# Kernel optimization log

Measured on AMD Instinct MI355X. Metric: run time of the kernel, lower is better.

## Reference

```python
import jax, jax.numpy as jnp
import numpy as np

B, C, N, M = 16, 256, 4096, 1024
EPS = 1e-5


def geometry_disentangle(x, num_select):
    # x: [B, C, N]. Variation score = L2 norm of mean-centered feature per point.
    score = jnp.linalg.norm(x - x.mean(axis=2, keepdims=True), axis=1)  # [B, N]
    _, idx_s = jax.lax.top_k(score, num_select)    # sharp: highest variation
    _, idx_g = jax.lax.top_k(-score, num_select)   # gentle: lowest variation
    sharp = jnp.take_along_axis(x, idx_s[:, None, :], axis=2)   # [B, C, M]
    gentle = jnp.take_along_axis(x, idx_g[:, None, :], axis=2)  # [B, C, M]
    return sharp, gentle


def cross_attention(x, ctx, Wq, bq, Wk, bk, Wv, bv, Wo, bo):
    # x: [B, C, N], ctx: [B, M, C] -> [B, C, N]
    c = x.shape[1]
    q = jnp.einsum('bcn,dc->bdn', x, Wq) + bq[None, :, None]  # conv1x1 on x
    k = jnp.einsum('bmc,dc->bmd', ctx, Wk) + bk
    v = jnp.einsum('bmc,dc->bmd', ctx, Wv) + bv
    scores = jnp.einsum('bdn,bmd->bnm', q, k) / jnp.sqrt(jnp.asarray(c, x.dtype))
    attn = jax.nn.softmax(scores, axis=-1)                     # [B, N, M]
    y = jnp.einsum('bnm,bmd->bdn', attn, v)                    # [B, C, N]
    y = jnp.einsum('bdn,ed->ben', y, Wo) + bo[None, :, None]   # output conv1x1
    return x + y


def conv_bn_relu(h, Wf, bf, gamma, beta):
    # Conv1d(k=1) + BatchNorm1d (training-mode batch stats) + ReLU. h: [B, 2C, N]
    y = jnp.einsum('bcn,dc->bdn', h, Wf) + bf[None, :, None]   # [B, C, N]
    mu = y.mean(axis=(0, 2), keepdims=True)
    var = y.var(axis=(0, 2), keepdims=True)
    y = (y - mu) * jax.lax.rsqrt(var + EPS)
    y = y * gamma[None, :, None] + beta[None, :, None]
    return jax.nn.relu(y)


def setup_inputs() -> dict:
    key = jax.random.key(0)
    ks = jax.random.split(key, 20)
    s = 0.02

    def w(k, shape):
        return (jax.random.normal(k, shape, dtype=jnp.float32) * s)

    inp = {
        'x': jax.random.normal(ks[0], (B, C, N), dtype=jnp.float32),
        'num_select': M,
        # sharp attention params
        'Wq_s': w(ks[1], (C, C)), 'bq_s': jnp.zeros((C,), jnp.float32),
        'Wk_s': w(ks[2], (C, C)), 'bk_s': jnp.zeros((C,), jnp.float32),
        'Wv_s': w(ks[3], (C, C)), 'bv_s': jnp.zeros((C,), jnp.float32),
        'Wo_s': w(ks[4], (C, C)), 'bo_s': jnp.zeros((C,), jnp.float32),
        # gentle attention params
        'Wq_g': w(ks[5], (C, C)), 'bq_g': jnp.zeros((C,), jnp.float32),
        'Wk_g': w(ks[6], (C, C)), 'bk_g': jnp.zeros((C,), jnp.float32),
        'Wv_g': w(ks[7], (C, C)), 'bv_g': jnp.zeros((C,), jnp.float32),
        'Wo_g': w(ks[8], (C, C)), 'bo_g': jnp.zeros((C,), jnp.float32),
        # fuse: Conv1d(2C -> C) + BN
        'Wf': w(ks[9], (C, 2 * C)), 'bf': jnp.zeros((C,), jnp.float32),
        'gamma': jnp.ones((C,), jnp.float32), 'beta': jnp.zeros((C,), jnp.float32),
    }
    return inp


def reference(x, Wq_s, bq_s, Wk_s, bk_s, Wv_s, bv_s, Wo_s, bo_s,
              Wq_g, bq_g, Wk_g, bk_g, Wv_g, bv_g, Wo_g, bo_g,
              Wf, bf, gamma, beta, num_select):
    sharp, gentle = geometry_disentangle(x, num_select)
    y_s = cross_attention(x, sharp.transpose(0, 2, 1), Wq_s, bq_s, Wk_s, bk_s, Wv_s, bv_s, Wo_s, bo_s)
    y_g = cross_attention(x, gentle.transpose(0, 2, 1), Wq_g, bq_g, Wk_g, bk_g, Wv_g, bv_g, Wo_g, bo_g)
    h = jnp.concatenate([y_s, y_g], axis=1)  # [B, 2C, N]
    return conv_bn_relu(h, Wf, bf, gamma, beta)
```

## Files before the change

kernel.cpp:

```cpp
#include <hip/hip_runtime.h>

#define BB 16
#define CC 256
#define NN 4096
#define MM 1024
#define EPSV 1e-5f
#define SCALE (1.0f/16.0f)

#define OFF_MU    0
#define OFF_SCORE 4096
#define OFF_IDX   69632
#define OFF_U     102400
#define OFF_WVZ   167936
#define OFF_WF12  233472
#define OFF_BVZ   299008
#define OFF_BZ    299264
#define OFF_W16   299520
#define OFF_XG    430592
#define OFF_K16   2527744
#define OFF_VT16  4624896
#define OFF_Z     6722048
#define OFF_BN    23499264
#define FIXED_F   23499776

typedef __attribute__((ext_vector_type(8))) short s16x8;
typedef __attribute__((ext_vector_type(4))) float f32x4;

__device__ __forceinline__ unsigned short f2bf(float f) {
    unsigned int u = __float_as_uint(f);
    return (unsigned short)((u + 0x7FFFu + ((u >> 16) & 1u)) >> 16);
}
__device__ __forceinline__ float bf2f(unsigned short h) {
    return __uint_as_float(((unsigned int)h) << 16);
}

__global__ __launch_bounds__(256) void zero_bn_kernel(float* bn) {
    int t = threadIdx.x;
    bn[t] = 0.f; bn[t + CC] = 0.f;
}

__global__ __launch_bounds__(256) void zero_rsum_kernel(float* r) {
    r[blockIdx.x * 256 + threadIdx.x] = 0.f;
}

__global__ __launch_bounds__(256) void mean_kernel(const float* __restrict__ x, float* __restrict__ mu) {
    int c = blockIdx.x, b = blockIdx.y, t = threadIdx.x;
    const float4* p = (const float4*)(x + ((size_t)b * CC + c) * NN);
    float s = 0.f;
    for (int n = t; n < NN / 4; n += 256) { float4 v = p[n]; s += (v.x + v.y) + (v.z + v.w); }
    __shared__ float red[256];
    red[t] = s; __syncthreads();
    for (int w = 128; w > 0; w >>= 1) { if (t < w) red[t] += red[t + w]; __syncthreads(); }
    if (t == 0) mu[b * CC + c] = red[0] * (1.0f / NN);
}

__global__ __launch_bounds__(256) void transpose_score_kernel(const float* __restrict__ x,
                                                              const float* __restrict__ mu,
                                                              unsigned short* __restrict__ xT,
                                                              float* __restrict__ score) {
    __shared__ float tile[32][33];
    __shared__ float smu[32];
    int b = blockIdx.z, c0 = blockIdx.y * 32, n0 = blockIdx.x * 32, t = threadIdx.x;
    int nl = t & 31, cr = t >> 5;
    if (t < 32) smu[t] = mu[b * CC + c0 + t];
#pragma unroll
    for (int q = 0; q < 4; ++q)
        tile[cr + q * 8][nl] = x[((size_t)b * CC + c0 + cr + q * 8) * NN + n0 + nl];
    __syncthreads();
    int nr = t >> 3, cq = t & 7;
    uint2 p;
    p.x = (unsigned int)f2bf(tile[cq * 4 + 0][nr]) | ((unsigned int)f2bf(tile[cq * 4 + 1][nr]) << 16);
    p.y = (unsigned int)f2bf(tile[cq * 4 + 2][nr]) | ((unsigned int)f2bf(tile[cq * 4 + 3][nr]) << 16);
    *(uint2*)&xT[((size_t)b * NN + n0 + nr) * CC + c0 + cq * 4] = p;
    int n = t & 31, cseg = t >> 5;
    float part = 0.f;
#pragma unroll
    for (int q = 0; q < 4; ++q) {
        float d = tile[cseg * 4 + q][n] - smu[cseg * 4 + q];
        part += d * d;
    }
    __syncthreads();
    tile[n][cseg] = part;
    __syncthreads();
    if (t < 32) {
        float s = 0.f;
#pragma unroll
        for (int j = 0; j < 8; ++j) s += tile[t][j];
        atomicAdd(&score[(size_t)b * NN + n0 + t], s);
    }
}

__global__ __launch_bounds__(1024) void select_kernel(const float* __restrict__ score,
                                                      int* __restrict__ idx_s, int* __restrict__ idx_g) {
    int b = blockIdx.x, t = threadIdx.x;
    __shared__ unsigned int keys[NN];
    __shared__ unsigned int hist[256];
    __shared__ unsigned int sbin, skrem;
    __shared__ int outcnt, eqcnt;
    __shared__ int eqidx[NN];
    for (int q = t; q < NN; q += 1024) keys[q] = __float_as_uint(score[(size_t)b * NN + q]);
    __syncthreads();
    for (int r = 0; r < 2; ++r) {
        unsigned int flip = r ? 0xFFFFFFFFu : 0u;
        unsigned int prefix = 0u, pmask = 0u;
        unsigned int k = MM;
        for (int pass = 0; pass < 4; ++pass) {
            int shift = 24 - 8 * pass;
            if (t < 256) hist[t] = 0u;
            __syncthreads();
            for (int q = t; q < NN; q += 1024) {
                unsigned int kv = keys[q] ^ flip;
                if ((kv & pmask) == prefix) atomicAdd(&hist[(kv >> shift) & 255u], 1u);
            }
            __syncthreads();
            for (int off = 1; off < 256; off <<= 1) {
                unsigned int v = 0u;
                if (t < 256) v = hist[t] + ((t + off < 256) ? hist[t + off] : 0u);
                __syncthreads();
                if (t < 256) hist[t] = v;
                __syncthreads();
            }
            if (t < 256) {
                unsigned int sj = hist[t], sj1 = (t < 255) ? hist[t + 1] : 0u;
                if (sj >= k && sj1 < k) { sbin = (unsigned int)t; skrem = k - sj1; }
            }
            __syncthreads();
            prefix |= sbin << shift;
            pmask |= 0xFFu << shift;
            k = skrem;
            __syncthreads();
        }
        unsigned int T = prefix;
        unsigned int krem = k;
        int* outp = r ? idx_g : idx_s;
        if (t == 0) { outcnt = 0; eqcnt = 0; }
        __syncthreads();
        for (int q = t; q < NN; q += 1024) {
            unsigned int kv = keys[q] ^ flip;
            if (kv > T) { int pp = atomicAdd(&outcnt, 1); outp[(size_t)b * MM + pp] = q; }
            else if (kv == T) { int pp = atomicAdd(&eqcnt, 1); eqidx[pp] = q; }
        }
        __syncthreads();
        int ne = eqcnt;
        for (int i = t; i < ne; i += 1024) {
            int me = eqidx[i];
            int rank = 0;
            for (int j = 0; j < ne; ++j) rank += (eqidx[j] < me) ? 1 : 0;
            if (rank < (int)krem) { int pp = atomicAdd(&outcnt, 1); outp[(size_t)b * MM + pp] = me; }
        }
        __syncthreads();
    }
}

__global__ __launch_bounds__(256) void smallmm_kernel(const float* __restrict__ A, int lda, int aoff,
                                                      const float* __restrict__ Bm, float* __restrict__ Cm) {
    int e = blockIdx.x, t = threadIdx.x;
    __shared__ float arow[CC];
    arow[t] = A[e * lda + aoff + t];
    __syncthreads();
    float acc = 0.f;
    for (int k = 0; k < CC; ++k) acc += arow[k] * Bm[k * CC + t];
    Cm[e * CC + t] = acc;
}

__global__ __launch_bounds__(256) void bvz_kernel(const float* __restrict__ U, const float* __restrict__ bv,
                                                  float* __restrict__ bvz) {
    int e = threadIdx.x;
    float acc = 0.f;
    for (int d = 0; d < CC; ++d) acc += U[e * CC + d] * bv[d];
    bvz[e] = acc;
}

__global__ __launch_bounds__(256) void bz_kernel(const float* __restrict__ Wf, const float* __restrict__ bf,
                                                 const float* __restrict__ bo_s, const float* __restrict__ bo_g,
                                                 float* __restrict__ bz) {
    int e = threadIdx.x;
    float acc = bf[e];
    for (int c = 0; c < CC; ++c)
        acc += Wf[e * 2 * CC + c] * bo_s[c] + Wf[e * 2 * CC + CC + c] * bo_g[c];
    bz[e] = acc;
}

__global__ __launch_bounds__(256) void wf12_kernel(const float* __restrict__ Wf, float* __restrict__ Wf12) {
    int e = blockIdx.x, c = threadIdx.x;
    Wf12[e * CC + c] = Wf[e * 2 * CC + c] + Wf[e * 2 * CC + CC + c];
}

__global__ __launch_bounds__(256) void conv_bf16_kernel(const float* __restrict__ src,
                                                        unsigned short* __restrict__ dst) {
    int i = blockIdx.x * 256 + threadIdx.x;
    float4 v = *(const float4*)(src + (size_t)i * 4);
    uint2 p;
    p.x = (unsigned int)f2bf(v.x) | ((unsigned int)f2bf(v.y) << 16);
    p.y = (unsigned int)f2bf(v.z) | ((unsigned int)f2bf(v.w) << 16);
    *(uint2*)&dst[(size_t)i * 4] = p;
}

__global__ __launch_bounds__(256) void gather_kernel(const unsigned short* __restrict__ xT,
                                                     const int* __restrict__ idx,
                                                     unsigned short* __restrict__ Xg) {
    int row = blockIdx.x * 4 + (threadIdx.x >> 6);
    int l = threadIdx.x & 63;
    int b = row >> 10, m = row & (MM - 1);
    int src = idx[b * MM + m];
    *(uint2*)&Xg[(size_t)row * CC + l * 4] =
        *(const uint2*)&xT[((size_t)b * NN + src) * CC + l * 4];
}

template<int OMODE>
__global__ __launch_bounds__(256, 3) void gemm_bt(
    const unsigned short* __restrict__ A, size_t a_bs,
    const unsigned short* __restrict__ Bw, size_t b_bs,
    const float* __restrict__ bias,
    void* __restrict__ outp, size_t o_bs, int ldo)
{
    __shared__ __align__(16) unsigned short As[128 * 32];
    __shared__ __align__(16) unsigned short Bs[128 * 32];
    int z = blockIdx.z;
    const unsigned short* Ab = A + z * a_bs + (size_t)blockIdx.x * 128 * CC;
    const unsigned short* Bb = Bw + z * b_bs + (size_t)blockIdx.y * 128 * CC;
    int t = threadIdx.x, w = t >> 6, l = t & 63, g = l >> 4, c16 = l & 15;
    int wi = w >> 1, wj = w & 1;
    int srow = t >> 2, skq = (t & 3) * 8;

    f32x4 acc[4][4];
#pragma unroll
    for (int a = 0; a < 4; ++a)
#pragma unroll
        for (int bq = 0; bq < 4; ++bq) acc[a][bq] = (f32x4){0.f, 0.f, 0.f, 0.f};

    for (int ks = 0; ks < 8; ++ks) {
        int k0 = ks * 32;
        uint4 a0 = *(const uint4*)(Ab + (size_t)srow * CC + k0 + skq);
        uint4 a1 = *(const uint4*)(Ab + (size_t)(srow + 64) * CC + k0 + skq);
        uint4 b0 = *(const uint4*)(Bb + (size_t)srow * CC + k0 + skq);
        uint4 b1 = *(const uint4*)(Bb + (size_t)(srow + 64) * CC + k0 + skq);
        __syncthreads();
        *(uint4*)&As[srow * 32 + skq] = a0;
        *(uint4*)&As[(srow + 64) * 32 + skq] = a1;
        *(uint4*)&Bs[srow * 32 + skq] = b0;
        *(uint4*)&Bs[(srow + 64) * 32 + skq] = b1;
        __syncthreads();
        s16x8 af[4], bf4[4];
#pragma unroll
        for (int fi = 0; fi < 4; ++fi)
            af[fi] = *(const s16x8*)&As[(wi * 64 + fi * 16 + c16) * 32 + g * 8];
#pragma unroll
        for (int fj = 0; fj < 4; ++fj)
            bf4[fj] = *(const s16x8*)&Bs[(wj * 64 + fj * 16 + c16) * 32 + g * 8];
#pragma unroll
        for (int fi = 0; fi < 4; ++fi)
#pragma unroll
            for (int fj = 0; fj < 4; ++fj)
                acc[fi][fj] = __builtin_amdgcn_mfma_f32_16x16x32_bf16(af[fi], bf4[fj], acc[fi][fj], 0, 0, 0);
    }

    int i0 = blockIdx.x * 128 + wi * 64, j0 = blockIdx.y * 128 + wj * 64;
#pragma unroll
    for (int fi = 0; fi < 4; ++fi) {
#pragma unroll
        for (int fj = 0; fj < 4; ++fj) {
            int colg = j0 + fj * 16 + c16;
#pragma unroll
            for (int r = 0; r < 4; ++r) {
                int rowg = i0 + fi * 16 + g * 4 + r;
                float v = acc[fi][fj][r] + (OMODE == 2 ? bias[rowg] : bias[colg]);
                if (OMODE == 0)
                    ((float*)outp)[z * o_bs + (size_t)rowg * ldo + colg] = v;
                else
                    ((unsigned short*)outp)[z * o_bs + (size_t)rowg * ldo + colg] = f2bf(v);
            }
        }
    }
}

__global__ __attribute__((amdgpu_flat_work_group_size(512, 512)))
__attribute__((amdgpu_waves_per_eu(2, 2)))
void fused_attn(
    const unsigned short* __restrict__ Q,
    const unsigned short* __restrict__ K,
    const unsigned short* __restrict__ Vt,
    float* __restrict__ Z)
{
    extern __shared__ __align__(16) unsigned char smem[];
    unsigned char* Ps = smem + 131072;
    float* rsl = (float*)(smem + 147456);

    int z = blockIdx.z;
    int n0 = blockIdx.x * 128;
    int t = threadIdx.x, w = t >> 6, l = t & 63, g = l >> 4, c16 = l & 15;
    int wn = w >> 1, wc = w & 1;

    const unsigned short* Qb = Q + ((size_t)z * NN + n0) * CC;
    const char* Kzb = (const char*)(K + (size_t)z * MM * CC);
    const char* Vzb = (const char*)(Vt + (size_t)z * CC * MM);

    s16x8 q[2][8];
#pragma unroll
    for (int fi = 0; fi < 2; ++fi)
#pragma unroll
        for (int ks = 0; ks < 8; ++ks)
            q[fi][ks] = *(const s16x8*)&Qb[(size_t)(wn * 32 + fi * 16 + c16) * CC + ks * 32 + g * 8];

    f32x4 o[2][8];
#pragma unroll
    for (int fi = 0; fi < 2; ++fi)
#pragma unroll
        for (int fj = 0; fj < 8; ++fj) o[fi][fj] = (f32x4){0.f, 0.f, 0.f, 0.f};
    float rs[2][4];
#pragma unroll
    for (int fi = 0; fi < 2; ++fi)
#pragma unroll
        for (int r = 0; r < 4; ++r) rs[fi][r] = 0.f;

    auto issueK = [&](int buf, int m0) {
#pragma unroll
        for (int j = 0; j < 4; ++j) {
            int cid = w * 4 + j;
            int row = cid * 2 + (l >> 5);
            int srcoff = ((l & 31) * 16) ^ ((row & 7) << 4);
            const char* gp = Kzb + (size_t)(m0 + row) * 512 + srcoff;
            __builtin_amdgcn_global_load_lds(
                (const __attribute__((address_space(1))) void*)gp,
                (__attribute__((address_space(3))) void*)(smem + buf * 32768 + cid * 1024),
                16, 0, 0);
        }
    };
    auto issueV = [&](int buf, int m0) {
#pragma unroll
        for (int j = 0; j < 4; ++j) {
            int cid = w * 4 + j;
            int row = cid * 8 + (l >> 3);
            int srcoff = ((l & 7) * 16) ^ ((row & 7) << 4);
            const char* gp = Vzb + (size_t)row * 2048 + (size_t)m0 * 2 + srcoff;
            __builtin_amdgcn_global_load_lds(
                (const __attribute__((address_space(1))) void*)gp,
                (__attribute__((address_space(3))) void*)(smem + 65536 + buf * 32768 + cid * 1024),
                16, 0, 0);
        }
    };

    issueK(0, 0);
    issueV(0, 0);

    for (int mt = 0; mt < 16; ++mt) {
        int cur = mt & 1;
        asm volatile("s_waitcnt vmcnt(0)" ::: "memory");
        __builtin_amdgcn_s_barrier();
        __builtin_amdgcn_sched_barrier(0);
        if (mt < 15) {
            issueK(1 - cur, (mt + 1) * 64);
            issueV(1 - cur, (mt + 1) * 64);
        }
        __builtin_amdgcn_sched_barrier(0);
        const unsigned char* Ks = smem + cur * 32768;
        const unsigned char* Vs = smem + 65536 + cur * 32768;

        f32x4 sacc[2][2];
#pragma unroll
        for (int fi = 0; fi < 2; ++fi)
#pragma unroll
            for (int fj = 0; fj < 2; ++fj) sacc[fi][fj] = (f32x4){0.f, 0.f, 0.f, 0.f};
        __builtin_amdgcn_s_setprio(1);
#pragma unroll
        for (int ks = 0; ks < 8; ++ks) {
            s16x8 kf[2];
#pragma unroll
            for (int fj = 0; fj < 2; ++fj) {
                int mr = wc * 32 + fj * 16 + c16;
                kf[fj] = *(const s16x8*)(Ks + ((mr * 512 + ks * 64 + g * 16) ^ ((mr & 7) << 4)));
            }
#pragma unroll
            for (int fi = 0; fi < 2; ++fi)
#pragma unroll
                for (int fj = 0; fj < 2; ++fj)
                    sacc[fi][fj] = __builtin_amdgcn_mfma_f32_16x16x32_bf16(q[fi][ks], kf[fj], sacc[fi][fj], 0, 0, 0);
        }
        __builtin_amdgcn_s_setprio(0);
#pragma unroll
        for (int fi = 0; fi < 2; ++fi)
#pragma unroll
            for (int fj = 0; fj < 2; ++fj)
#pragma unroll
                for (int r = 0; r < 4; ++r) {
                    float e = __expf(sacc[fi][fj][r] * SCALE);
                    unsigned short h = f2bf(e);
                    int nr = wn * 32 + fi * 16 + g * 4 + r;
                    int mc = wc * 32 + fj * 16 + c16;
                    *(unsigned short*)(Ps + ((nr * 128 + mc * 2) ^ ((nr & 7) << 4))) = h;
                    rs[fi][r] += bf2f(h);
                }
        asm volatile("s_waitcnt lgkmcnt(0)" ::: "memory");
        __builtin_amdgcn_s_barrier();
        __builtin_amdgcn_sched_barrier(0);
        __builtin_amdgcn_s_setprio(1);
#pragma unroll
        for (int ks2 = 0; ks2 < 2; ++ks2) {
            s16x8 pa[2];
#pragma unroll
            for (int fi = 0; fi < 2; ++fi) {
                int nr = wn * 32 + fi * 16 + c16;
                pa[fi] = *(const s16x8*)(Ps + ((nr * 128 + ks2 * 64 + g * 16) ^ ((nr & 7) << 4)));
            }
#pragma unroll
            for (int fj = 0; fj < 8; ++fj) {
                int er = wc * 128 + fj * 16 + c16;
                s16x8 vb = *(const s16x8*)(Vs + ((er * 128 + ks2 * 64 + g * 16) ^ ((er & 7) << 4)));
#pragma unroll
                for (int fi = 0; fi < 2; ++fi)
                    o[fi][fj] = __builtin_amdgcn_mfma_f32_16x16x32_bf16(pa[fi], vb, o[fi][fj], 0, 0, 0);
            }
        }
        __builtin_amdgcn_s_setprio(0);
    }

#pragma unroll
    for (int fi = 0; fi < 2; ++fi)
#pragma unroll
        for (int r = 0; r < 4; ++r) {
            float v = rs[fi][r];
            v += __shfl_xor(v, 1); v += __shfl_xor(v, 2);
            v += __shfl_xor(v, 4); v += __shfl_xor(v, 8);
            if (c16 == 0) rsl[wc * 128 + wn * 32 + fi * 16 + g * 4 + r] = v;
        }
    __syncthreads();
    float* Zb = Z + ((size_t)z * NN + n0) * CC;
#pragma unroll
    for (int fi = 0; fi < 2; ++fi)
#pragma unroll
        for (int r = 0; r < 4; ++r) {
            int nr = wn * 32 + fi * 16 + g * 4 + r;
            float inv = 1.0f / (rsl[nr] + rsl[128 + nr]);
#pragma unroll
            for (int fj = 0; fj < 8; ++fj) {
                int e = wc * 128 + fj * 16 + c16;
                Zb[(size_t)nr * CC + e] += o[fi][fj][r] * inv;
            }
        }
}

__global__ __launch_bounds__(256) void bn_stats_kernel(const float* __restrict__ Z, float* __restrict__ bn) {
    int blk = blockIdx.x, e = threadIdx.x;
    const float* p = Z + (size_t)blk * 256 * CC + e;
    float s1 = 0.f, s2 = 0.f;
    for (int r = 0; r < 256; ++r) { float v = p[(size_t)r * CC]; s1 += v; s2 += v * v; }
    atomicAdd(&bn[e], s1);
    atomicAdd(&bn[CC + e], s2);
}

__global__ __launch_bounds__(256) void bn_apply_kernel(const float* __restrict__ Z, const float* __restrict__ bn,
                                                       const float* __restrict__ gamma, const float* __restrict__ beta,
                                                       float* __restrict__ out) {
    int b = blockIdx.z, e0 = blockIdx.y * 32, n0 = blockIdx.x * 32, t = threadIdx.x;
    __shared__ float tile[32][33];
    int c = t & 31, r0 = (t >> 5) * 4;
#pragma unroll
    for (int q = 0; q < 4; ++q)
        tile[r0 + q][c] = Z[((size_t)b * NN + n0 + r0 + q) * CC + e0 + c];
    __syncthreads();
    int n = t & 31, er0 = (t >> 5) * 4;
    const float invcnt = 1.0f / (BB * NN);
#pragma unroll
    for (int q = 0; q < 4; ++q) {
        int e = e0 + er0 + q;
        float mean = bn[e] * invcnt;
        float var = bn[CC + e] * invcnt - mean * mean;
        float rsq = rsqrtf(var + EPSV);
        float v = (tile[n][er0 + q] - mean) * rsq * gamma[e] + beta[e];
        out[((size_t)b * CC + e) * NN + n0 + n] = fmaxf(v, 0.f);
    }
}

extern "C" void kernel_launch(void* const* d_in, const int* in_sizes, int n_in,
                              void* d_out, int out_size, void* d_ws, size_t ws_size,
                              hipStream_t stream) {
    const float* x    = (const float*)d_in[0];
    const float* Wq_s = (const float*)d_in[2];  const float* bq_s = (const float*)d_in[3];
    const float* Wk_s = (const float*)d_in[4];  const float* bk_s = (const float*)d_in[5];
    const float* Wv_s = (const float*)d_in[6];  const float* bv_s = (const float*)d_in[7];
    const float* Wo_s = (const float*)d_in[8];  const float* bo_s = (const float*)d_in[9];
    const float* Wq_g = (const float*)d_in[10]; const float* bq_g = (const float*)d_in[11];
    const float* Wk_g = (const float*)d_in[12]; const float* bk_g = (const float*)d_in[13];
    const float* Wv_g = (const float*)d_in[14]; const float* bv_g = (const float*)d_in[15];
    const float* Wo_g = (const float*)d_in[16]; const float* bo_g = (const float*)d_in[17];
    const float* Wf   = (const float*)d_in[18]; const float* bf   = (const float*)d_in[19];
    const float* gamma = (const float*)d_in[20]; const float* beta = (const float*)d_in[21];

    float* ws    = (float*)d_ws;
    float* mu    = ws + OFF_MU;
    float* score = ws + OFF_SCORE;
    int*   idx_s = (int*)(ws + OFF_IDX);
    int*   idx_g = idx_s + BB * MM;
    float* U     = ws + OFF_U;
    float* Wvz   = ws + OFF_WVZ;
    float* Wf12  = ws + OFF_WF12;
    float* bvz   = ws + OFF_BVZ;
    float* bz    = ws + OFF_BZ;
    unsigned short* Wf12_16 = (unsigned short*)(ws + OFF_W16);
    unsigned short* Wq16    = Wf12_16 + 65536;
    unsigned short* Wk16    = Wq16 + 65536;
    unsigned short* Wvz16   = Wk16 + 65536;
    unsigned short* Xg16 = (unsigned short*)(ws + OFF_XG);
    unsigned short* K16  = (unsigned short*)(ws + OFF_K16);
    unsigned short* Vt16 = (unsigned short*)(ws + OFF_VT16);
    float* Z     = ws + OFF_Z;
    float* bn    = ws + OFF_BN;
    unsigned short* Q16  = (unsigned short*)d_out;
    unsigned short* xT16 = Q16 + (size_t)BB * NN * CC;

    zero_bn_kernel<<<1, 256, 0, stream>>>(bn);
    mean_kernel<<<dim3(CC, BB), 256, 0, stream>>>(x, mu);
    zero_rsum_kernel<<<BB * NN / 256, 256, 0, stream>>>(score);
    transpose_score_kernel<<<dim3(NN / 32, CC / 32, BB), 256, 0, stream>>>(x, mu, xT16, score);
    select_kernel<<<BB, 1024, 0, stream>>>(score, idx_s, idx_g);
    wf12_kernel<<<CC, 256, 0, stream>>>(Wf, Wf12);
    bz_kernel<<<1, 256, 0, stream>>>(Wf, bf, bo_s, bo_g, bz);
    conv_bf16_kernel<<<64, 256, 0, stream>>>(Wf12, Wf12_16);
    gemm_bt<0><<<dim3(512, 2, 1), 256, 0, stream>>>(xT16, 0, Wf12_16, 0, bz, Z, 0, CC);

    for (int br = 0; br < 2; ++br) {
        const float* Wo = br ? Wo_g : Wo_s;
        const float* Wv = br ? Wv_g : Wv_s;  const float* bv = br ? bv_g : bv_s;
        const float* Wk = br ? Wk_g : Wk_s;  const float* bk = br ? bk_g : bk_s;
        const float* Wq = br ? Wq_g : Wq_s;  const float* bq = br ? bq_g : bq_s;
        int* idx = br ? idx_g : idx_s;
        int aoff = br ? CC : 0;
        smallmm_kernel<<<CC, 256, 0, stream>>>(Wf, 2 * CC, aoff, Wo, U);
        smallmm_kernel<<<CC, 256, 0, stream>>>(U, CC, 0, Wv, Wvz);
        bvz_kernel<<<1, 256, 0, stream>>>(U, bv, bvz);
        conv_bf16_kernel<<<64, 256, 0, stream>>>(Wq, Wq16);
        conv_bf16_kernel<<<64, 256, 0, stream>>>(Wk, Wk16);
        conv_bf16_kernel<<<64, 256, 0, stream>>>(Wvz, Wvz16);
        gather_kernel<<<BB * MM / 4, 256, 0, stream>>>(xT16, idx, Xg16);
        gemm_bt<1><<<dim3(BB * MM / 128, 2, 1), 256, 0, stream>>>(Xg16, 0, Wk16, 0, bk, K16, 0, CC);
        gemm_bt<2><<<dim3(2, 8, BB), 256, 0, stream>>>(Wvz16, 0, Xg16, (size_t)MM * CC, bvz,
                                                       Vt16, (size_t)CC * MM, MM);
        gemm_bt<1><<<dim3(512, 2, 1), 256, 0, stream>>>(xT16, 0, Wq16, 0, bq, Q16, 0, CC);

        fused_attn<<<dim3(NN / 128, 1, BB), 512, 148480, stream>>>(Q16, K16, Vt16, Z);
    }

    bn_stats_kernel<<<BB * NN / 256, 256, 0, stream>>>(Z, bn);
    bn_apply_kernel<<<dim3(NN / 32, CC / 32, BB), 256, 0, stream>>>(Z, bn, gamma, beta, (float*)d_out);
}
```

Baseline: 624.1 us.

## Software-pipeline attention: overlap next-tile QK/exp with current PV using rotating buffers

The fused attention loop now works on 32-key tiles instead of 64. Each iteration computes QK^T and exp for the next tile while doing the P·V MFMAs for the current one. K is double-buffered, V triple-buffered and P double-buffered in LDS, so only one barrier per iteration is needed instead of two, and LDS use drops from about 148KB to about 116KB. The cost is twice as many iterations with smaller MFMA batches per step. Correctness also depends on __syncthreads waiting for the outstanding global_load_lds transfers, which the old code enforced with an explicit vmcnt wait.

```diff
diff --git a/kernel.cpp b/kernel.cpp
--- a/kernel.cpp
+++ b/kernel.cpp
@@ -283,8 +283,7 @@
     float* __restrict__ Z)
 {
     extern __shared__ __align__(16) unsigned char smem[];
-    unsigned char* Ps = smem + 131072;
-    float* rsl = (float*)(smem + 147456);
+    float* rsl = (float*)(smem + 114688);
 
     int z = blockIdx.z;
     int n0 = blockIdx.x * 128;
@@ -315,103 +314,94 @@
 
     auto issueK = [&](int buf, int m0) {
 #pragma unroll
-        for (int j = 0; j < 4; ++j) {
-            int cid = w * 4 + j;
+        for (int j = 0; j < 2; ++j) {
+            int cid = w * 2 + j;
             int row = cid * 2 + (l >> 5);
             int srcoff = ((l & 31) * 16) ^ ((row & 7) << 4);
             const char* gp = Kzb + (size_t)(m0 + row) * 512 + srcoff;
             __builtin_amdgcn_global_load_lds(
                 (const __attribute__((address_space(1))) void*)gp,
-                (__attribute__((address_space(3))) void*)(smem + buf * 32768 + cid * 1024),
+                (__attribute__((address_space(3))) void*)(smem + buf * 16384 + cid * 1024),
                 16, 0, 0);
         }
     };
-    auto issueV = [&](int buf, int m0) {
-#pragma unroll
-        for (int j = 0; j < 4; ++j) {
-            int cid = w * 4 + j;
-            int row = cid * 8 + (l >> 3);
-            int srcoff = ((l & 7) * 16) ^ ((row & 7) << 4);
+    auto issueV = [&](int slot, int m0) {
+#pragma unroll
+        for (int j = 0; j < 2; ++j) {
+            int cid = w * 2 + j;
+            int row = cid * 16 + (l >> 2);
+            int srcoff = ((l & 3) * 16) ^ ((row & 3) << 4);
             const char* gp = Vzb + (size_t)row * 2048 + (size_t)m0 * 2 + srcoff;
             __builtin_amdgcn_global_load_lds(
                 (const __attribute__((address_space(1))) void*)gp,
-                (__attribute__((address_space(3))) void*)(smem + 65536 + buf * 32768 + cid * 1024),
+                (__attribute__((address_space(3))) void*)(smem + 32768 + slot * 16384 + cid * 1024),
                 16, 0, 0);
         }
     };
 
-    issueK(0, 0);
-    issueV(0, 0);
-
-    for (int mt = 0; mt < 16; ++mt) {
-        int cur = mt & 1;
-        asm volatile("s_waitcnt vmcnt(0)" ::: "memory");
-        __builtin_amdgcn_s_barrier();
+    auto qk_exp = [&](int buf, int par) {
+        const unsigned char* Ks = smem + buf * 16384;
+        unsigned char* Ps = smem + 81920 + par * 16384;
+        f32x4 sacc[2];
+#pragma unroll
+        for (int fi = 0; fi < 2; ++fi) sacc[fi] = (f32x4){0.f, 0.f, 0.f, 0.f};
+        int mr = wc * 16 + c16;
+        __builtin_amdgcn_s_setprio(1);
+#pragma unroll
+        for (int ks = 0; ks < 8; ++ks) {
+            s16x8 kf = *(const s16x8*)(Ks + ((mr * 512 + ks * 64 + g * 16) ^ ((mr & 7) << 4)));
+#pragma unroll
+            for (int fi = 0; fi < 2; ++fi)
+                sacc[fi] = __builtin_amdgcn_mfma_f32_16x16x32_bf16(q[fi][ks], kf, sacc[fi], 0, 0, 0);
+        }
+        __builtin_amdgcn_s_setprio(0);
+        int mc = wc * 16 + c16;
+#pragma unroll
+        for (int fi = 0; fi < 2; ++fi)
+#pragma unroll
+            for (int r = 0; r < 4; ++r) {
+                float e = __expf(sacc[fi][r] * SCALE);
+                unsigned short h = f2bf(e);
+                int nr = wn * 32 + fi * 16 + g * 4 + r;
+                *(unsigned short*)(Ps + ((nr * 128 + mc * 2) ^ ((nr & 7) << 4))) = h;
+                rs[fi][r] += bf2f(h);
+            }
+    };
+    auto pv = [&](int slot, int par) {
+        const unsigned char* Vs = smem + 32768 + slot * 16384;
+        const unsigned char* Ps = smem + 81920 + par * 16384;
+        s16x8 pa[2];
+#pragma unroll
+        for (int fi = 0; fi < 2; ++fi) {
+            int nr = wn * 32 + fi * 16 + c16;
+            pa[fi] = *(const s16x8*)(Ps + ((nr * 128 + g * 16) ^ ((nr & 7) << 4)));
+        }
+        __builtin_amdgcn_s_setprio(1);
+#pragma unroll
+        for (int fj = 0; fj < 8; ++fj) {
+            int er = wc * 128 + fj * 16 + c16;
+            s16x8 vb = *(const s16x8*)(Vs + ((er * 64 + g * 16) ^ ((er & 3) << 4)));
+#pragma unroll
+            for (int fi = 0; fi < 2; ++fi)
+                o[fi][fj] = __builtin_amdgcn_mfma_f32_16x16x32_bf16(pa[fi], vb, o[fi][fj], 0, 0, 0);
+        }
+        __builtin_amdgcn_s_setprio(0);
+    };
+
+    issueK(0, 0); issueV(0, 0);
+    issueK(1, 32); issueV(1, 32);
+    __syncthreads();
+    qk_exp(0, 0);
+
+    for (int mt = 0; mt < 32; ++mt) {
+        __syncthreads();
+        if (mt < 30) {
+            issueK(mt & 1, (mt + 2) * 32);
+            issueV((mt + 2) % 3, (mt + 2) * 32);
+        }
         __builtin_amdgcn_sched_barrier(0);
-        if (mt < 15) {
-            issueK(1 - cur, (mt + 1) * 64);
-            issueV(1 - cur, (mt + 1) * 64);
-        }
-        __builtin_amdgcn_sched_barrier(0);
-        const unsigned char* Ks = smem + cur * 32768;
-        const unsigned char* Vs = smem + 65536 + cur * 32768;
-
-        f32x4 sacc[2][2];
-#pragma unroll
-        for (int fi = 0; fi < 2; ++fi)
-#pragma unroll
-            for (int fj = 0; fj < 2; ++fj) sacc[fi][fj] = (f32x4){0.f, 0.f, 0.f, 0.f};
-        __builtin_amdgcn_s_setprio(1);
-#pragma unroll
-        for (int ks = 0; ks < 8; ++ks) {
-            s16x8 kf[2];
-#pragma unroll
-            for (int fj = 0; fj < 2; ++fj) {
-                int mr = wc * 32 + fj * 16 + c16;
-                kf[fj] = *(const s16x8*)(Ks + ((mr * 512 + ks * 64 + g * 16) ^ ((mr & 7) << 4)));
-            }
-#pragma unroll
-            for (int fi = 0; fi < 2; ++fi)
-#pragma unroll
-                for (int fj = 0; fj < 2; ++fj)
-                    sacc[fi][fj] = __builtin_amdgcn_mfma_f32_16x16x32_bf16(q[fi][ks], kf[fj], sacc[fi][fj], 0, 0, 0);
-        }
-        __builtin_amdgcn_s_setprio(0);
-#pragma unroll
-        for (int fi = 0; fi < 2; ++fi)
-#pragma unroll
-            for (int fj = 0; fj < 2; ++fj)
-#pragma unroll
-                for (int r = 0; r < 4; ++r) {
-                    float e = __expf(sacc[fi][fj][r] * SCALE);
-                    unsigned short h = f2bf(e);
-                    int nr = wn * 32 + fi * 16 + g * 4 + r;
-                    int mc = wc * 32 + fj * 16 + c16;
-                    *(unsigned short*)(Ps + ((nr * 128 + mc * 2) ^ ((nr & 7) << 4))) = h;
-                    rs[fi][r] += bf2f(h);
-                }
-        asm volatile("s_waitcnt lgkmcnt(0)" ::: "memory");
-        __builtin_amdgcn_s_barrier();
-        __builtin_amdgcn_sched_barrier(0);
-        __builtin_amdgcn_s_setprio(1);
-#pragma unroll
-        for (int ks2 = 0; ks2 < 2; ++ks2) {
-            s16x8 pa[2];
-#pragma unroll
-            for (int fi = 0; fi < 2; ++fi) {
-                int nr = wn * 32 + fi * 16 + c16;
-                pa[fi] = *(const s16x8*)(Ps + ((nr * 128 + ks2 * 64 + g * 16) ^ ((nr & 7) << 4)));
-            }
-#pragma unroll
-            for (int fj = 0; fj < 8; ++fj) {
-                int er = wc * 128 + fj * 16 + c16;
-                s16x8 vb = *(const s16x8*)(Vs + ((er * 128 + ks2 * 64 + g * 16) ^ ((er & 7) << 4)));
-#pragma unroll
-                for (int fi = 0; fi < 2; ++fi)
-                    o[fi][fj] = __builtin_amdgcn_mfma_f32_16x16x32_bf16(pa[fi], vb, o[fi][fj], 0, 0, 0);
-            }
-        }
-        __builtin_amdgcn_s_setprio(0);
+        if (mt < 31) qk_exp((mt + 1) & 1, (mt + 1) & 1);
+        pv(mt % 3, mt & 1);
     }
 
 #pragma unroll
@@ -537,7 +527,7 @@
                                                        Vt16, (size_t)CC * MM, MM);
         gemm_bt<1><<<dim3(512, 2, 1), 256, 0, stream>>>(xT16, 0, Wq16, 0, bq, Q16, 0, CC);
 
-        fused_attn<<<dim3(NN / 128, 1, BB), 512, 148480, stream>>>(Q16, K16, Vt16, Z);
+        fused_attn<<<dim3(NN / 128, 1, BB), 512, 115712, stream>>>(Q16, K16, Vt16, Z);
     }
 
     bn_stats_kernel<<<BB * NN / 256, 256, 0, stream>>>(Z, bn);
```

Measured after the change: 630.7 us. Within noise of the previous version (+1.1%).
